# Performance work log

Measured on AMD Instinct MI355X. Metric: run time of the kernel, lower is better.

Reference implementation:

```python
import jax, jax.numpy as jnp
import numpy as np

V, E, H, B, TE, TD = 32000, 256, 256, 32, 128, 64


def _gru_cell(x, h, Wi, Wh, bi, bh):
    # PyTorch GRU gate order: r, z, n
    gi = x @ Wi.T + bi            # [B, 3H]
    gh = h @ Wh.T + bh            # [B, 3H]
    i_r, i_z, i_n = jnp.split(gi, 3, axis=-1)
    h_r, h_z, h_n = jnp.split(gh, 3, axis=-1)
    r = jax.nn.sigmoid(i_r + h_r)
    z = jax.nn.sigmoid(i_z + h_z)
    n = jnp.tanh(i_n + r * h_n)
    return (1.0 - z) * n + z * h


def _run_gru(x_seq, h0, Wi, Wh, bi, bh, reverse=False):
    # x_seq: [B, T, D] -> outputs [B, T, H]
    xs = jnp.swapaxes(x_seq, 0, 1)  # [T, B, D]
    def step(h, x_t):
        h = _gru_cell(x_t, h, Wi, Wh, bi, bh)
        return h, h
    _, ys = jax.lax.scan(step, h0, xs, reverse=reverse)
    return jnp.swapaxes(ys, 0, 1)


def setup_inputs() -> dict:
    key = jax.random.key(0)
    ks = jax.random.split(key, 22)
    k = 1.0 / np.sqrt(H)
    u = lambda kk, shape, a: jax.random.uniform(kk, shape, jnp.float32, -a, a)
    return {
        'enc_in': jax.random.randint(ks[0], (B, TE), 0, V),
        'dec_in': jax.random.randint(ks[1], (B, TD), 0, V),
        'embed_W': u(ks[2], (V, E), 0.1),
        'Wi_f': u(ks[3], (3 * H, E), k), 'Wh_f': u(ks[4], (3 * H, H), k),
        'bi_f': u(ks[5], (3 * H,), k), 'bh_f': u(ks[6], (3 * H,), k),
        'Wi_b': u(ks[7], (3 * H, E), k), 'Wh_b': u(ks[8], (3 * H, H), k),
        'bi_b': u(ks[9], (3 * H,), k), 'bh_b': u(ks[10], (3 * H,), k),
        'Wi_d': u(ks[11], (3 * H, E + 2 * H), k), 'Wh_d': u(ks[12], (3 * H, H), k),
        'bi_d': u(ks[13], (3 * H,), k), 'bh_d': u(ks[14], (3 * H,), k),
        'W1_w': u(ks[15], (H, 2 * H), 1.0 / np.sqrt(2 * H)), 'W1_b': u(ks[16], (H,), 1.0 / np.sqrt(2 * H)),
        'W2_w': u(ks[17], (2 * H, H), k), 'W2_b': u(ks[18], (2 * H,), k),
        'lin_w': u(ks[19], (V, H), 0.1), 'lin_b': jnp.zeros((V,), jnp.float32),
    }


def reference(enc_in, dec_in, embed_W, Wi_f, Wh_f, bi_f, bh_f, Wi_b, Wh_b, bi_b, bh_b,
              Wi_d, Wh_d, bi_d, bh_d, W1_w, W1_b, W2_w, W2_b, lin_w, lin_b):
    # ---- encoder (bidirectional GRU, 1 layer) ----
    enc_emb = embed_W[enc_in]                                   # [B, TE, E]
    h0 = jnp.zeros((B, H), enc_emb.dtype)
    out_f = _run_gru(enc_emb, h0, Wi_f, Wh_f, bi_f, bh_f)       # [B, TE, H]
    out_b = _run_gru(enc_emb, h0, Wi_b, Wh_b, bi_b, bh_b, reverse=True)
    encoded = jnp.concatenate([out_f, out_b], axis=-1)          # [B, TE, 2H]

    # last valid state per example: encoded[i, sizes[i]-1]
    sizes = (enc_in > 0).sum(axis=1)                            # [B]
    last_states = encoded[jnp.arange(B), sizes - 1]             # [B, 2H]

    # ---- decoder with Luong attention (teacher forcing) ----
    dec_emb = embed_W[dec_in]                                   # [B, TD, E]
    h_init = last_states @ W1_w.T + W1_b                        # [B, H]
    ctx_init = jnp.zeros((B, 2 * H), enc_emb.dtype)

    def dec_step(carry, x_t):
        h, ctx = carry
        inp = jnp.concatenate([ctx, x_t], axis=-1)              # [B, E+2H]
        h = _gru_cell(inp, h, Wi_d, Wh_d, bi_d, bh_d)           # [B, H]
        comp = h @ W2_w.T + W2_b                                # [B, 2H]
        scores = jax.nn.softmax(jnp.einsum('bte,be->bt', encoded, comp), axis=-1)
        ctx = jnp.einsum('bt,bte->be', scores, encoded)          # [B, 2H]
        return (h, ctx), h

    _, outs = jax.lax.scan(dec_step, (h_init, ctx_init), jnp.swapaxes(dec_emb, 0, 1))
    outs = jnp.swapaxes(outs, 0, 1)                             # [B, TD, H]
    logits = outs @ lin_w.T + lin_b                             # [B, TD, V]
    return logits
```

## Files before the change

### kernel.cpp

```cpp
#include <hip/hip_runtime.h>
#include <hip/hip_bf16.h>

#define Vv 32000
#define Ee 256
#define Hh 256
#define Bb 32
#define TEe 128
#define TDd 64

typedef __attribute__((ext_vector_type(4))) float f32x4;
typedef __attribute__((ext_vector_type(8))) short short8;
typedef __attribute__((ext_vector_type(2))) unsigned int uint2v;
typedef __attribute__((ext_vector_type(4))) unsigned int uint4v;

static __device__ __forceinline__ unsigned short f2bf(float f){
  unsigned u = __float_as_uint(f);
  u += 0x7fffu + ((u >> 16) & 1u);
  return (unsigned short)(u >> 16);
}
static __device__ __forceinline__ unsigned pack2(float a, float b){
  return ((unsigned)f2bf(b) << 16) | (unsigned)f2bf(a);
}
static __device__ __forceinline__ float dot8(uint4v u, const float* hh){
  float s = 0.f;
  #pragma unroll
  for (int i = 0; i < 4; ++i){
    unsigned w = u[i];
    s = fmaf(__uint_as_float(w << 16),        hh[2*i],   s);
    s = fmaf(__uint_as_float(w & 0xffff0000u), hh[2*i+1], s);
  }
  return s;
}
static __device__ __forceinline__ float sigmoidf_(float x){
  return 1.f / (1.f + __expf(-x));
}

__global__ void k_sizes(const int* __restrict__ enc_in, int* __restrict__ sizes){
  int b = threadIdx.x;
  if (b < Bb){
    int c = 0;
    for (int t = 0; t < TEe; ++t) c += (enc_in[b*TEe + t] > 0);
    sizes[b] = c;
  }
}

__global__ void k_gather(const int* __restrict__ tok, const float* __restrict__ embW,
                         unsigned short* __restrict__ out, int rows){
  int i = blockIdx.x * 256 + threadIdx.x;
  int r = i >> 8, c = i & 255;
  if (r < rows) out[i] = f2bf(embW[(size_t)tok[r]*Ee + c]);
}

__global__ void k_chunkw(const float* __restrict__ src, unsigned short* __restrict__ dst, int rows){
  int idx = blockIdx.x * 256 + threadIdx.x;
  if (idx < rows * 256){
    int i = idx & 7, r = (idx >> 3) % rows, kb = idx / (rows * 8);
    dst[idx] = f2bf(src[(size_t)r*256 + kb*8 + i]);
  }
}

__global__ void k_convert(const float* __restrict__ Wi_f, const float* __restrict__ Wi_b,
                          const float* __restrict__ Wi_d, const float* __restrict__ W2_w,
                          unsigned short* __restrict__ wif, unsigned short* __restrict__ wib,
                          unsigned short* __restrict__ wid, unsigned short* __restrict__ w2t){
  int idx = blockIdx.x * 256 + threadIdx.x;
  if (idx < 196608)        wif[idx] = f2bf(Wi_f[idx]);
  else if (idx < 393216)   wib[idx - 196608] = f2bf(Wi_b[idx - 196608]);
  else if (idx < 983040)   wid[idx - 393216] = f2bf(Wi_d[idx - 393216]);
  else if (idx < 1114112){
    int l = idx - 983040;
    int n = l >> 9, k = l & 511;
    w2t[l] = f2bf(W2_w[k*256 + n]);
  }
}

__global__ void k_projchunk(const unsigned short* __restrict__ in, unsigned short* __restrict__ out){
  int idx = blockIdx.x * 256 + threadIdx.x;
  int i = idx & 7;
  int t1 = idx >> 3;
  int n = t1 % 768;
  int t2 = t1 / 768;
  int kb = t2 & 15, b = t2 >> 4;
  out[idx] = in[(size_t)(b*TEe + kb*8 + i)*768 + n];
}

template<bool A_BF16, bool B_BF16, bool B_KMAJOR, bool OUT_BF16>
__global__ __launch_bounds__(256) void k_gemm(
  const void* __restrict__ Av, const void* __restrict__ Bv,
  const float* __restrict__ bias, void* __restrict__ Cv,
  int M, int N, int K, int lda, int ldb, int ldc)
{
  __shared__ unsigned short lA[128*40];
  __shared__ unsigned short lB[128*40];
  const int tid  = threadIdx.x;
  const int lane = tid & 63;
  const int w = tid >> 6, wr = w >> 1, wc = w & 1;
  const int m0 = blockIdx.y * 128, n0 = blockIdx.x * 128;
  f32x4 acc[4][4];
  #pragma unroll
  for (int i = 0; i < 4; ++i)
    #pragma unroll
    for (int j = 0; j < 4; ++j) acc[i][j] = (f32x4){0.f,0.f,0.f,0.f};

  for (int k0 = 0; k0 < K; k0 += 32){
    if (A_BF16){
      const unsigned short* A = (const unsigned short*)Av;
      #pragma unroll
      for (int it = 0; it < 2; ++it){
        int idx = tid + it*256; int r = idx >> 2, q = idx & 3;
        *(uint4v*)&lA[r*40 + q*8] = *(const uint4v*)(A + (size_t)(m0+r)*lda + k0 + q*8);
      }
    } else {
      const float* A = (const float*)Av;
      #pragma unroll
      for (int it = 0; it < 4; ++it){
        int idx = tid + it*256; int r = idx >> 3, q = idx & 7;
        f32x4 v = *(const f32x4*)(A + (size_t)(m0+r)*lda + k0 + q*4);
        uint2v pk; pk[0] = pack2(v[0], v[1]); pk[1] = pack2(v[2], v[3]);
        *(uint2v*)&lA[r*40 + q*4] = pk;
      }
    }
    if (B_KMAJOR){
      const float* Bp = (const float*)Bv;
      #pragma unroll
      for (int it = 0; it < 4; ++it){
        int idx = tid + it*256; int kk = idx >> 5, nq = idx & 31;
        f32x4 v = *(const f32x4*)(Bp + (size_t)(k0+kk)*ldb + n0 + nq*4);
        #pragma unroll
        for (int s2 = 0; s2 < 4; ++s2) lB[(nq*4+s2)*40 + kk] = f2bf(v[s2]);
      }
    } else if (B_BF16){
      const unsigned short* Bp = (const unsigned short*)Bv;
      #pragma unroll
      for (int it = 0; it < 2; ++it){
        int idx = tid + it*256; int r = idx >> 2, q = idx & 3;
        *(uint4v*)&lB[r*40 + q*8] = *(const uint4v*)(Bp + (size_t)(n0+r)*ldb + k0 + q*8);
      }
    } else {
      const float* Bp = (const float*)Bv;
      #pragma unroll
      for (int it = 0; it < 4; ++it){
        int idx = tid + it*256; int r = idx >> 3, q = idx & 7;
        f32x4 v = *(const f32x4*)(Bp + (size_t)(n0+r)*ldb + k0 + q*4);
        uint2v pk; pk[0] = pack2(v[0], v[1]); pk[1] = pack2(v[2], v[3]);
        *(uint2v*)&lB[r*40 + q*4] = pk;
      }
    }
    __syncthreads();
    short8 av[4], bv[4];
    #pragma unroll
    for (int i = 0; i < 4; ++i)
      av[i] = *(const short8*)&lA[(wr*64 + i*16 + (lane&15))*40 + (lane>>4)*8];
    #pragma unroll
    for (int j = 0; j < 4; ++j)
      bv[j] = *(const short8*)&lB[(wc*64 + j*16 + (lane&15))*40 + (lane>>4)*8];
    #pragma unroll
    for (int i = 0; i < 4; ++i)
      #pragma unroll
      for (int j = 0; j < 4; ++j)
        acc[i][j] = __builtin_amdgcn_mfma_f32_16x16x32_bf16(av[i], bv[j], acc[i][j], 0, 0, 0);
    __syncthreads();
  }
  #pragma unroll
  for (int i = 0; i < 4; ++i){
    #pragma unroll
    for (int j = 0; j < 4; ++j){
      int col = n0 + wc*64 + j*16 + (lane & 15);
      float bb = bias ? bias[col] : 0.f;
      #pragma unroll
      for (int r = 0; r < 4; ++r){
        int row = m0 + wr*64 + i*16 + (lane>>4)*4 + r;
        float v = acc[i][j][r] + bb;
        if (OUT_BF16) ((unsigned short*)Cv)[(size_t)row*ldc + col] = f2bf(v);
        else          ((float*)Cv)[(size_t)row*ldc + col] = v;
      }
    }
  }
}

__global__ __launch_bounds__(1024) void k_encoder(
  const unsigned short* __restrict__ Whf, const unsigned short* __restrict__ Whb,
  const float* __restrict__ bhf, const float* __restrict__ bhb,
  const float* __restrict__ gif, const float* __restrict__ gib,
  float* __restrict__ encoded, unsigned short* __restrict__ encoded_bf,
  const float* __restrict__ lin_w, unsigned short* __restrict__ lin_bf, int do_lin)
{
  if (blockIdx.x >= 64){
    if (do_lin){
      const int nlin = Vv*Hh;
      for (int i = (blockIdx.x - 64)*1024 + threadIdx.x; i < nlin; i += 128*1024)
        lin_bf[i] = f2bf(lin_w[i]);
    }
    return;
  }
  extern __shared__ char smem[];
  unsigned short* lw = (unsigned short*)smem;
  float* hA   = (float*)(smem + 131072);
  float* hB   = (float*)(smem + 132096);
  float* parA = (float*)(smem + 133120);
  float* parB = (float*)(smem + 137216);
  const int dir = blockIdx.x & 1, b = blockIdx.x >> 1;
  const unsigned short* Wh = dir ? Whb : Whf;
  const float* bh = dir ? bhb : bhf;
  const float* gi = dir ? gib : gif;
  const int T = threadIdx.x;
  const int rl = T & 255, q4 = T >> 8;
  const int rrh = T & 511, hf = T >> 9;
  const unsigned short* wsrc = Wh + (size_t)(hf*16)*6144 + (size_t)(256 + rrh)*8;
  uint4v wb[8];
  #pragma unroll
  for (int d = 0; d < 8; ++d) wb[d] = *(const uint4v*)(wsrc + (size_t)d*6144);
  for (int cc = T; cc < 256*32; cc += 1024){
    int r = cc >> 5, q = cc & 31;
    *(uint4v*)&lw[(r*32 + (q ^ (r & 31)))*8] = *(const uint4v*)(Wh + (size_t)q*6144 + r*8);
  }
  float bh0 = 0.f, bh1 = 0.f, bh2 = 0.f;
  if (T < 256){ bh0 = bh[T]; bh1 = bh[T+256]; bh2 = bh[T+512]; hA[T] = 0.f; }
  __syncthreads();
  const float* hc = hA; float* hn = hB;
  for (int s = 0; s < TEe; ++s){
    const int t = dir ? (TEe-1-s) : s;
    float aL = 0.f;
    #pragma unroll
    for (int i = 0; i < 8; ++i){
      const int ck = q4*8 + i;
      float hr[8];
      *(f32x4*)&hr[0] = *(const f32x4*)&hc[ck*8];
      *(f32x4*)&hr[4] = *(const f32x4*)&hc[ck*8+4];
      aL += dot8(*(const uint4v*)&lw[(rl*32 + (ck ^ (rl & 31)))*8], hr);
    }
    parA[q4*256 + rl] = aL;
    float aR = 0.f;
    const float* hh = hc + hf*128;
    #pragma unroll
    for (int q = 0; q < 16; ++q){
      float hr[8];
      *(f32x4*)&hr[0] = *(const f32x4*)&hh[q*8];
      *(f32x4*)&hr[4] = *(const f32x4*)&hh[q*8+4];
      aR += dot8(wb[q & 7], hr);
      wb[q & 7] = *(const uint4v*)(wsrc + (size_t)((q < 8) ? (q + 8) : (q - 8))*6144);
    }
    parB[hf*512 + rrh] = aR;
    __syncthreads();
    if (T < 256){
      const int j = T;
      const float* grow = gi + (size_t)(b*TEe + t)*768;
      const float A0 = parA[j] + parA[256+j] + parA[512+j] + parA[768+j] + bh0;
      const float A1 = parB[j] + parB[512+j] + bh1;
      const float A2 = parB[256+j] + parB[768+j] + bh2;
      const float r = sigmoidf_(grow[j] + A0);
      const float z = sigmoidf_(grow[j+256] + A1);
      const float n = tanhf(grow[j+512] + r*A2);
      const float hnew = (1.f - z)*n + z*hc[j];
      hn[j] = hnew;
      const size_t off = (size_t)(b*TEe + t)*512 + dir*256 + j;
      encoded[off] = hnew;
      encoded_bf[off] = f2bf(hnew);
    }
    __syncthreads();
    const float* tmp = hc; hc = hn; hn = (float*)tmp;
  }
}

__global__ void k_encb2(const float* __restrict__ encoded, const float* __restrict__ W2b,
                        float* __restrict__ encb2){
  int r = blockIdx.x, l = threadIdx.x;
  const float* e = encoded + (size_t)r*512;
  float s = 0.f;
  for (int k = l; k < 512; k += 64) s += e[k]*W2b[k];
  for (int off = 32; off; off >>= 1) s += __shfl_down(s, off);
  if (l == 0) encb2[r] = s;
}

__global__ void k_hinit(const float* __restrict__ encoded, const int* __restrict__ sizes,
                        const float* __restrict__ W1w, const float* __restrict__ W1b,
                        float* __restrict__ h0){
  int b = blockIdx.x, o = threadIdx.x;
  int idx = sizes[b] - 1;
  idx = idx < 0 ? 0 : (idx > TEe-1 ? TEe-1 : idx);
  const float* ls = encoded + (size_t)(b*TEe + idx)*512;
  const float* wv = W1w + (size_t)o*512;
  float s = W1b[o];
  for (int k = 0; k < 512; k += 4){
    f32x4 a = *(const f32x4*)(ls + k);
    f32x4 w4 = *(const f32x4*)(wv + k);
    s = fmaf(a[0],w4[0], fmaf(a[1],w4[1], fmaf(a[2],w4[2], fmaf(a[3],w4[3], s))));
  }
  h0[b*256 + o] = s;
}

#define DLR 128
__global__ __launch_bounds__(512, 1) void k_decoder(
  const unsigned short* __restrict__ Whd, const float* __restrict__ bhd,
  const float* __restrict__ gidx,
  const unsigned short* __restrict__ encw2,
  const float* __restrict__ encb2,
  const unsigned short* __restrict__ projt,
  const float* __restrict__ h0,
  unsigned short* __restrict__ outs_bf)
{
  extern __shared__ char smem[];
  unsigned short* le = (unsigned short*)smem;
  unsigned short* lw = (unsigned short*)(smem + 65536);
  float* h    = (float*)(smem + 131072);
  float* parL = (float*)(smem + 132096);
  float* parS1= (float*)(smem + 134144);
  float* parS2= (float*)(smem + 136192);
  float* gcs  = (float*)(smem + 138240);
  float* cpar = (float*)(smem + 140288);
  float* p    = (float*)(smem + 142336);
  float* ebl  = (float*)(smem + 142848);
  const int b = blockIdx.x, T = threadIdx.x;
  const unsigned short* ptc = projt + (size_t)b*98304;
  const unsigned short* wsrcM = Whd + (size_t)(DLR + T)*8;
  const int trow = 640 + (T >> 2), tq = (T & 3)*8;
  const unsigned short* wsrcT = Whd + (size_t)trow*8;
  const unsigned short* csrcM = ptc + (size_t)T*8;
  const int crow = 512 + (T >> 1), cq = (T & 1)*8;
  const unsigned short* csrcT = ptc + (size_t)crow*8;
  uint4v wb[8], wb2[2], cb[4], cb2[2];
  #pragma unroll
  for (int d = 0; d < 8; ++d) wb[d] = *(const uint4v*)(wsrcM + (size_t)d*6144);
  wb2[0] = *(const uint4v*)(wsrcT + (size_t)tq*6144);
  wb2[1] = *(const uint4v*)(wsrcT + (size_t)(tq+1)*6144);
  #pragma unroll
  for (int d = 0; d < 4; ++d) cb[d] = *(const uint4v*)(csrcM + (size_t)d*6144);
  cb2[0] = *(const uint4v*)(csrcT + (size_t)cq*6144);
  cb2[1] = *(const uint4v*)(csrcT + (size_t)(cq+1)*6144);
  for (int cc = T; cc < 128*32; cc += 512){
    int r = cc >> 5, q = cc & 31;
    *(uint4v*)&le[(r*32 + (q ^ (r & 31)))*8] =
        *(const uint4v*)(encw2 + ((size_t)(b*TEe + r) << 8) + (q << 3));
  }
  for (int cc = T; cc < DLR*32; cc += 512){
    int r = cc >> 5, q = cc & 31;
    *(uint4v*)&lw[(r*32 + (q ^ (r & 31)))*8] =
        *(const uint4v*)(Whd + (size_t)q*6144 + r*8);
  }
  for (int i = T; i < 256; i += 512) h[i] = h0[b*256 + i];
  gcs[T] = 0.f; cpar[T] = 0.f;
  if (T < TEe) ebl[T] = encb2[b*TEe + T];
  float bh0 = 0.f, bh1 = 0.f, bh2 = 0.f;
  if (T < 256){ bh0 = bhd[T]; bh1 = bhd[T+256]; bh2 = bhd[T+512]; }
  __syncthreads();
  float g0 = 0.f, g1 = 0.f, g2 = 0.f;
  if (T < 256){
    const float* grow = gidx + (size_t)(b*TDd)*768;
    g0 = grow[T]; g1 = grow[T+256]; g2 = grow[T+512];
  }
  #define DOTS_BODY                                                            \
  {                                                                            \
    { const int rL2 = T >> 2, qb2 = (T & 3)*8;                                 \
      const unsigned short* lwr = lw + rL2*256;                                \
      float a = 0.f;                                                           \
      _Pragma("unroll")                                                        \
      for (int i = 0; i < 8; ++i){                                             \
        const int q = qb2 + i;                                                 \
        float hr[8];                                                           \
        *(f32x4*)&hr[0] = *(const f32x4*)&h[q*8];                              \
        *(f32x4*)&hr[4] = *(const f32x4*)&h[q*8+4];                            \
        a += dot8(*(const uint4v*)(lwr + ((q ^ (rL2 & 31)) << 3)), hr);        \
      }                                                                        \
      parL[(T & 3)*128 + rL2] = a;                                             \
    }                                                                          \
    { float a = 0.f;                                                           \
      _Pragma("unroll")                                                        \
      for (int q = 0; q < 32; ++q){                                            \
        float hr[8];                                                           \
        *(f32x4*)&hr[0] = *(const f32x4*)&h[q*8];                              \
        *(f32x4*)&hr[4] = *(const f32x4*)&h[q*8+4];                            \
        a += dot8(wb[q & 7], hr);                                              \
        wb[q & 7] = *(const uint4v*)(wsrcM + (size_t)((q < 24) ? (q + 8) : (q - 24))*6144); \
      }                                                                        \
      parS1[T] = a;                                                            \
    }                                                                          \
    { float a = 0.f;                                                           \
      _Pragma("unroll")                                                        \
      for (int i = 0; i < 8; ++i){                                             \
        const int q = tq + i;                                                  \
        float hr[8];                                                           \
        *(f32x4*)&hr[0] = *(const f32x4*)&h[q*8];                              \
        *(f32x4*)&hr[4] = *(const f32x4*)&h[q*8+4];                            \
        a += dot8(wb2[i & 1], hr);                                             \
        wb2[i & 1] = *(const uint4v*)(wsrcT + (size_t)(tq + ((i < 6) ? (i + 2) : (i - 6)))*6144); \
      }                                                                        \
      parS2[(T & 3)*128 + (T >> 2)] = a;                                       \
    }                                                                          \
  }
  DOTS_BODY
  __syncthreads();
  for (int t = 0; t < TDd; ++t){
    if (T < 256){
      const int j = T;
      float A0, A2;
      if (j < 128){
        A0 = parL[j] + parL[128+j] + parL[256+j] + parL[384+j];
        A2 = parS1[384+j];
      } else {
        A0 = parS1[j-128];
        A2 = parS2[j-128] + parS2[j] + parS2[j+128] + parS2[j+256];
      }
      const float A1 = parS1[128+j];
      const float gcr = gcs[j];
      const float gcz = gcs[256+j];
      const float gcn = cpar[j] + cpar[256+j];
      const float r = sigmoidf_(g0 + gcr + A0 + bh0);
      const float z = sigmoidf_(g1 + gcz + A1 + bh1);
      const float n = tanhf(g2 + gcn + r*(A2 + bh2));
      const float hnew = (1.f - z)*n + z*h[j];
      h[j] = hnew;
      outs_bf[(size_t)(b*TDd + t)*256 + j] = f2bf(hnew);
    }
    if (t + 1 == TDd) break;
    __syncthreads();
    if (T < 256){
      const float* grow = gidx + (size_t)(b*TDd + t + 1)*768;
      g0 = grow[T]; g1 = grow[T+256]; g2 = grow[T+512];
    }
    DOTS_BODY
    {
      const int pos = T >> 2, kq = (T & 3)*8;
      const unsigned short* er = le + pos*256;
      float s = 0.f;
      #pragma unroll
      for (int i = 0; i < 8; ++i){
        const int q = kq + i;
        float hr[8];
        *(f32x4*)&hr[0] = *(const f32x4*)&h[q*8];
        *(f32x4*)&hr[4] = *(const f32x4*)&h[q*8+4];
        s += dot8(*(const uint4v*)(er + ((q ^ (pos & 31)) << 3)), hr);
      }
      s += __shfl_xor(s, 1);
      s += __shfl_xor(s, 2);
      if ((T & 3) == 0) p[pos] = s + ebl[pos];
    }
    __syncthreads();
    if (T < 64){
      float m = fmaxf(p[T], p[T+64]);
      for (int off = 32; off; off >>= 1) m = fmaxf(m, __shfl_xor(m, off));
      float e0 = __expf(p[T] - m), e1 = __expf(p[T+64] - m);
      float ss = e0 + e1;
      for (int off = 32; off; off >>= 1) ss += __shfl_xor(ss, off);
      float inv = 1.f / ss;
      p[T] = e0*inv; p[T+64] = e1*inv;
    }
    __syncthreads();
    {
      float c = 0.f;
      #pragma unroll
      for (int q = 0; q < 16; ++q){
        float pr[8];
        *(f32x4*)&pr[0] = *(const f32x4*)&p[q*8];
        *(f32x4*)&pr[4] = *(const f32x4*)&p[q*8+4];
        c += dot8(cb[q & 3], pr);
        cb[q & 3] = *(const uint4v*)(csrcM + (size_t)((q < 12) ? (q + 4) : (q - 12))*6144);
      }
      gcs[T] = c;
      float c2 = 0.f;
      #pragma unroll
      for (int i = 0; i < 8; ++i){
        const int q = cq + i;
        float pr[8];
        *(f32x4*)&pr[0] = *(const f32x4*)&p[q*8];
        *(f32x4*)&pr[4] = *(const f32x4*)&p[q*8+4];
        c2 += dot8(cb2[i & 1], pr);
        cb2[i & 1] = *(const uint4v*)(csrcT + (size_t)(cq + ((i < 6) ? (i + 2) : (i - 6)))*6144);
      }
      cpar[(T & 1)*256 + (T >> 1)] = c2;
    }
    __syncthreads();
  }
  #undef DOTS_BODY
}

extern "C" void kernel_launch(void* const* d_in, const int* in_sizes, int n_in,
                              void* d_out, int out_size, void* d_ws, size_t ws_size,
                              hipStream_t stream)
{
  (void)in_sizes; (void)n_in; (void)out_size;
  const int*   enc_in = (const int*)d_in[0];
  const int*   dec_in = (const int*)d_in[1];
  const float* embW   = (const float*)d_in[2];
  const float* Wi_f   = (const float*)d_in[3];
  const float* Wh_f   = (const float*)d_in[4];
  const float* bi_f   = (const float*)d_in[5];
  const float* bh_f   = (const float*)d_in[6];
  const float* Wi_b   = (const float*)d_in[7];
  const float* Wh_b   = (const float*)d_in[8];
  const float* bi_b   = (const float*)d_in[9];
  const float* bh_b   = (const float*)d_in[10];
  const float* Wi_d   = (const float*)d_in[11];
  const float* Wh_d   = (const float*)d_in[12];
  const float* bi_d   = (const float*)d_in[13];
  const float* bh_d   = (const float*)d_in[14];
  const float* W1_w   = (const float*)d_in[15];
  const float* W1_b   = (const float*)d_in[16];
  const float* W2_w   = (const float*)d_in[17];
  const float* W2_b   = (const float*)d_in[18];
  const float* lin_w  = (const float*)d_in[19];
  const float* lin_b  = (const float*)d_in[20];

  char* scr = (char*)d_out;
  unsigned short* emb_enc = (unsigned short*)(scr + 0);
  unsigned short* emb_dec = (unsigned short*)(scr + 2097152);
  float* gi_f    = (float*)(scr + 3145728);
  float* gi_b    = (float*)(scr + 15728640);
  float* gi_dx   = (float*)(scr + 28311552);
  float* enc     = (float*)(scr + 34603008);
  unsigned short* enc_bf  = (unsigned short*)(scr + 42991616);
  unsigned short* projf_bf= (unsigned short*)(scr + 47185920);
  unsigned short* whf_bf = (unsigned short*)(scr + 53477376);
  unsigned short* whb_bf = (unsigned short*)(scr + 53870592);
  unsigned short* whd_bf = (unsigned short*)(scr + 54263808);
  unsigned short* encw2  = (unsigned short*)(scr + 54657024);
  unsigned short* projt  = (unsigned short*)(scr + 56754176);
  unsigned short* wif_bf = (unsigned short*)(scr + 63045632);
  unsigned short* wib_bf = (unsigned short*)(scr + 63438848);
  unsigned short* wid_bf = (unsigned short*)(scr + 63832064);
  unsigned short* w2t_bf = (unsigned short*)(scr + 65011712);
  float* encb2 = (float*)(scr + 65273856);
  int*   sizes = (int*)(scr + 65290240);
  float* h0    = (float*)(scr + 65290368);

  unsigned short* outs_bf = (unsigned short*)d_ws;
  unsigned short* lin_bf  = (unsigned short*)((char*)d_ws + (1<<20));
  const bool big = ws_size >= (size_t)(1<<20) + 16384000u + 1024u;

  hipFuncSetAttribute((const void*)k_encoder, hipFuncAttributeMaxDynamicSharedMemorySize, 141312);
  hipFuncSetAttribute((const void*)k_decoder, hipFuncAttributeMaxDynamicSharedMemorySize, 143360);

  k_sizes<<<1, 32, 0, stream>>>(enc_in, sizes);
  k_gather<<<Bb*TEe, 256, 0, stream>>>(enc_in, embW, emb_enc, Bb*TEe);
  k_gather<<<Bb*TDd, 256, 0, stream>>>(dec_in, embW, emb_dec, Bb*TDd);
  k_chunkw<<<768, 256, 0, stream>>>(Wh_f, whf_bf, 768);
  k_chunkw<<<768, 256, 0, stream>>>(Wh_b, whb_bf, 768);
  k_chunkw<<<768, 256, 0, stream>>>(Wh_d, whd_bf, 768);
  k_convert<<<4352, 256, 0, stream>>>(Wi_f, Wi_b, Wi_d, W2_w, wif_bf, wib_bf, wid_bf, w2t_bf);

  k_gemm<true,true,false,false><<<dim3(6,32), 256, 0, stream>>>(
      emb_enc, wif_bf, bi_f, gi_f, 4096, 768, 256, 256, 256, 768);
  k_gemm<true,true,false,false><<<dim3(6,32), 256, 0, stream>>>(
      emb_enc, wib_bf, bi_b, gi_b, 4096, 768, 256, 256, 256, 768);
  k_gemm<true,true,false,false><<<dim3(6,16), 256, 0, stream>>>(
      emb_dec, wid_bf + 512, bi_d, gi_dx, 2048, 768, 256, 256, 768, 768);

  k_encoder<<<192, 1024, 141312, stream>>>(whf_bf, whb_bf, bh_f, bh_b, gi_f, gi_b,
                                           enc, enc_bf, lin_w, lin_bf, big ? 1 : 0);
  k_encb2<<<Bb*TEe, 64, 0, stream>>>(enc, W2_b, encb2);

  k_gemm<true,true,false,true><<<dim3(2,32), 256, 0, stream>>>(
      enc_bf, w2t_bf, nullptr, encw2, 4096, 256, 512, 512, 512, 256);
  k_gemm<true,true,false,true><<<dim3(6,32), 256, 0, stream>>>(
      enc_bf, wid_bf, nullptr, projf_bf, 4096, 768, 512, 512, 768, 768);
  k_projchunk<<<(Bb*16*768*8)/256, 256, 0, stream>>>(projf_bf, projt);
  k_hinit<<<Bb, 256, 0, stream>>>(enc, sizes, W1_w, W1_b, h0);

  k_decoder<<<Bb, 512, 143360, stream>>>(whd_bf, bh_d, gi_dx, encw2, encb2, projt, h0, outs_bf);

  if (big)
    k_gemm<true,true,false,false><<<dim3(250,16), 256, 0, stream>>>(
        outs_bf, lin_bf, lin_b, d_out, 2048, 32000, 256, 256, 256, 32000);
  else
    k_gemm<true,false,false,false><<<dim3(250,16), 256, 0, stream>>>(
        outs_bf, lin_w, lin_b, d_out, 2048, 32000, 256, 256, 256, 32000);
}
```

Measured before the change: 1.650 ms.

## Fuse prep kernels, embedding gather into GEMM, and chunked projection output

Measured after the change: 1.624 ms, median of 2. No clear change (-1.6%).

```diff
diff --git a/kernel.cpp b/kernel.cpp
--- a/kernel.cpp
+++ b/kernel.cpp
@@ -35,58 +35,35 @@
   return 1.f / (1.f + __expf(-x));
 }
 
-__global__ void k_sizes(const int* __restrict__ enc_in, int* __restrict__ sizes){
-  int b = threadIdx.x;
-  if (b < Bb){
-    int c = 0;
-    for (int t = 0; t < TEe; ++t) c += (enc_in[b*TEe + t] > 0);
-    sizes[b] = c;
-  }
-}
-
-__global__ void k_gather(const int* __restrict__ tok, const float* __restrict__ embW,
-                         unsigned short* __restrict__ out, int rows){
-  int i = blockIdx.x * 256 + threadIdx.x;
-  int r = i >> 8, c = i & 255;
-  if (r < rows) out[i] = f2bf(embW[(size_t)tok[r]*Ee + c]);
-}
-
-__global__ void k_chunkw(const float* __restrict__ src, unsigned short* __restrict__ dst, int rows){
+__global__ void k_prep(const float* __restrict__ Wh_f, const float* __restrict__ Wh_b,
+                       const float* __restrict__ Wh_d,
+                       const float* __restrict__ Wi_f, const float* __restrict__ Wi_b,
+                       const float* __restrict__ Wi_d, const float* __restrict__ W2_w,
+                       unsigned short* __restrict__ whf, unsigned short* __restrict__ whb,
+                       unsigned short* __restrict__ whd,
+                       unsigned short* __restrict__ wif, unsigned short* __restrict__ wib,
+                       unsigned short* __restrict__ wid, unsigned short* __restrict__ w2t){
   int idx = blockIdx.x * 256 + threadIdx.x;
-  if (idx < rows * 256){
-    int i = idx & 7, r = (idx >> 3) % rows, kb = idx / (rows * 8);
-    dst[idx] = f2bf(src[(size_t)r*256 + kb*8 + i]);
-  }
-}
-
-__global__ void k_convert(const float* __restrict__ Wi_f, const float* __restrict__ Wi_b,
-                          const float* __restrict__ Wi_d, const float* __restrict__ W2_w,
-                          unsigned short* __restrict__ wif, unsigned short* __restrict__ wib,
-                          unsigned short* __restrict__ wid, unsigned short* __restrict__ w2t){
-  int idx = blockIdx.x * 256 + threadIdx.x;
-  if (idx < 196608)        wif[idx] = f2bf(Wi_f[idx]);
-  else if (idx < 393216)   wib[idx - 196608] = f2bf(Wi_b[idx - 196608]);
-  else if (idx < 983040)   wid[idx - 393216] = f2bf(Wi_d[idx - 393216]);
-  else if (idx < 1114112){
-    int l = idx - 983040;
+  if (idx < 589824){
+    int which = idx / 196608, local = idx % 196608;
+    int i = local & 7, r = (local >> 3) % 768, kb = local / 6144;
+    const float* src = (which == 0) ? Wh_f : (which == 1) ? Wh_b : Wh_d;
+    unsigned short* dst = (which == 0) ? whf : (which == 1) ? whb : whd;
+    dst[local] = f2bf(src[(size_t)r*256 + kb*8 + i]);
+  } else if (idx < 786432)   wif[idx - 589824] = f2bf(Wi_f[idx - 589824]);
+  else if (idx < 983040)     wib[idx - 786432] = f2bf(Wi_b[idx - 786432]);
+  else if (idx < 1572864)    wid[idx - 983040] = f2bf(Wi_d[idx - 983040]);
+  else if (idx < 1703936){
+    int l = idx - 1572864;
     int n = l >> 9, k = l & 511;
     w2t[l] = f2bf(W2_w[k*256 + n]);
   }
 }
 
-__global__ void k_projchunk(const unsigned short* __restrict__ in, unsigned short* __restrict__ out){
-  int idx = blockIdx.x * 256 + threadIdx.x;
-  int i = idx & 7;
-  int t1 = idx >> 3;
-  int n = t1 % 768;
-  int t2 = t1 / 768;
-  int kb = t2 & 15, b = t2 >> 4;
-  out[idx] = in[(size_t)(b*TEe + kb*8 + i)*768 + n];
-}
-
-template<bool A_BF16, bool B_BF16, bool B_KMAJOR, bool OUT_BF16>
+template<bool A_BF16, bool A_GATHER, bool B_BF16, int OUTMODE>
 __global__ __launch_bounds__(256) void k_gemm(
-  const void* __restrict__ Av, const void* __restrict__ Bv,
+  const void* __restrict__ Av, const int* __restrict__ tokp, const float* __restrict__ embp,
+  const void* __restrict__ Bv,
   const float* __restrict__ bias, void* __restrict__ Cv,
   int M, int N, int K, int lda, int ldb, int ldc)
 {
@@ -103,7 +80,16 @@
     for (int j = 0; j < 4; ++j) acc[i][j] = (f32x4){0.f,0.f,0.f,0.f};
 
   for (int k0 = 0; k0 < K; k0 += 32){
-    if (A_BF16){
+    if (A_GATHER){
+      #pragma unroll
+      for (int it = 0; it < 4; ++it){
+        int idx = tid + it*256; int r = idx >> 3, q = idx & 7;
+        const float* src = embp + (size_t)tokp[m0 + r]*256 + k0 + q*4;
+        f32x4 v = *(const f32x4*)src;
+        uint2v pk; pk[0] = pack2(v[0], v[1]); pk[1] = pack2(v[2], v[3]);
+        *(uint2v*)&lA[r*40 + q*4] = pk;
+      }
+    } else if (A_BF16){
       const unsigned short* A = (const unsigned short*)Av;
       #pragma unroll
       for (int it = 0; it < 2; ++it){
@@ -120,16 +106,7 @@
         *(uint2v*)&lA[r*40 + q*4] = pk;
       }
     }
-    if (B_KMAJOR){
-      const float* Bp = (const float*)Bv;
-      #pragma unroll
-      for (int it = 0; it < 4; ++it){
-        int idx = tid + it*256; int kk = idx >> 5, nq = idx & 31;
-        f32x4 v = *(const f32x4*)(Bp + (size_t)(k0+kk)*ldb + n0 + nq*4);
-        #pragma unroll
-        for (int s2 = 0; s2 < 4; ++s2) lB[(nq*4+s2)*40 + kk] = f2bf(v[s2]);
-      }
-    } else if (B_BF16){
+    if (B_BF16){
       const unsigned short* Bp = (const unsigned short*)Bv;
       #pragma unroll
       for (int it = 0; it < 2; ++it){
@@ -171,8 +148,14 @@
       for (int r = 0; r < 4; ++r){
         int row = m0 + wr*64 + i*16 + (lane>>4)*4 + r;
         float v = acc[i][j][r] + bb;
-        if (OUT_BF16) ((unsigned short*)Cv)[(size_t)row*ldc + col] = f2bf(v);
-        else          ((float*)Cv)[(size_t)row*ldc + col] = v;
+        if (OUTMODE == 2){
+          ((unsigned short*)Cv)[(size_t)(row >> 7)*98304 + (size_t)((row & 127) >> 3)*6144
+                                + (size_t)col*8 + (row & 7)] = f2bf(v);
+        } else if (OUTMODE == 1){
+          ((unsigned short*)Cv)[(size_t)row*ldc + col] = f2bf(v);
+        } else {
+          ((float*)Cv)[(size_t)row*ldc + col] = v;
+        }
       }
     }
   }
@@ -220,6 +203,11 @@
   const float* hc = hA; float* hn = hB;
   for (int s = 0; s < TEe; ++s){
     const int t = dir ? (TEe-1-s) : s;
+    float g0 = 0.f, g1 = 0.f, g2 = 0.f;
+    if (T < 256){
+      const float* grow = gi + (size_t)(b*TEe + t)*768;
+      g0 = grow[T]; g1 = grow[T+256]; g2 = grow[T+512];
+    }
     float aL = 0.f;
     #pragma unroll
     for (int i = 0; i < 8; ++i){
@@ -244,13 +232,12 @@
     __syncthreads();
     if (T < 256){
       const int j = T;
-      const float* grow = gi + (size_t)(b*TEe + t)*768;
       const float A0 = parA[j] + parA[256+j] + parA[512+j] + parA[768+j] + bh0;
       const float A1 = parB[j] + parB[512+j] + bh1;
       const float A2 = parB[256+j] + parB[768+j] + bh2;
-      const float r = sigmoidf_(grow[j] + A0);
-      const float z = sigmoidf_(grow[j+256] + A1);
-      const float n = tanhf(grow[j+512] + r*A2);
+      const float r = sigmoidf_(g0 + A0);
+      const float z = sigmoidf_(g1 + A1);
+      const float n = tanhf(g2 + r*A2);
       const float hnew = (1.f - z)*n + z*hc[j];
       hn[j] = hnew;
       const size_t off = (size_t)(b*TEe + t)*512 + dir*256 + j;
@@ -262,31 +249,34 @@
   }
 }
 
-__global__ void k_encb2(const float* __restrict__ encoded, const float* __restrict__ W2b,
-                        float* __restrict__ encb2){
-  int r = blockIdx.x, l = threadIdx.x;
-  const float* e = encoded + (size_t)r*512;
-  float s = 0.f;
-  for (int k = l; k < 512; k += 64) s += e[k]*W2b[k];
-  for (int off = 32; off; off >>= 1) s += __shfl_down(s, off);
-  if (l == 0) encb2[r] = s;
-}
-
-__global__ void k_hinit(const float* __restrict__ encoded, const int* __restrict__ sizes,
-                        const float* __restrict__ W1w, const float* __restrict__ W1b,
-                        float* __restrict__ h0){
-  int b = blockIdx.x, o = threadIdx.x;
-  int idx = sizes[b] - 1;
-  idx = idx < 0 ? 0 : (idx > TEe-1 ? TEe-1 : idx);
-  const float* ls = encoded + (size_t)(b*TEe + idx)*512;
-  const float* wv = W1w + (size_t)o*512;
-  float s = W1b[o];
-  for (int k = 0; k < 512; k += 4){
-    f32x4 a = *(const f32x4*)(ls + k);
-    f32x4 w4 = *(const f32x4*)(wv + k);
-    s = fmaf(a[0],w4[0], fmaf(a[1],w4[1], fmaf(a[2],w4[2], fmaf(a[3],w4[3], s))));
-  }
-  h0[b*256 + o] = s;
+__global__ __launch_bounds__(256) void k_post(
+  const float* __restrict__ encoded, const float* __restrict__ W2b, float* __restrict__ encb2,
+  const int* __restrict__ enc_in, const float* __restrict__ W1w, const float* __restrict__ W1b,
+  float* __restrict__ h0)
+{
+  if (blockIdx.x < 1024){
+    const int r = blockIdx.x*4 + (threadIdx.x >> 6), l = threadIdx.x & 63;
+    const float* e = encoded + (size_t)r*512;
+    float s = 0.f;
+    for (int k = l; k < 512; k += 64) s += e[k]*W2b[k];
+    for (int off = 32; off; off >>= 1) s += __shfl_down(s, off);
+    if (l == 0) encb2[r] = s;
+  } else {
+    const int b = blockIdx.x - 1024, o = threadIdx.x;
+    int c = 0;
+    for (int t = 0; t < TEe; ++t) c += (enc_in[b*TEe + t] > 0);
+    int idx = c - 1;
+    idx = idx < 0 ? 0 : (idx > TEe-1 ? TEe-1 : idx);
+    const float* ls = encoded + (size_t)(b*TEe + idx)*512;
+    const float* wv = W1w + (size_t)o*512;
+    float s = W1b[o];
+    for (int k = 0; k < 512; k += 4){
+      f32x4 a = *(const f32x4*)(ls + k);
+      f32x4 w4 = *(const f32x4*)(wv + k);
+      s = fmaf(a[0],w4[0], fmaf(a[1],w4[1], fmaf(a[2],w4[2], fmaf(a[3],w4[3], s))));
+    }
+    h0[b*256 + o] = s;
+  }
 }
 
 #define DLR 128
@@ -501,14 +491,11 @@
   const float* lin_b  = (const float*)d_in[20];
 
   char* scr = (char*)d_out;
-  unsigned short* emb_enc = (unsigned short*)(scr + 0);
-  unsigned short* emb_dec = (unsigned short*)(scr + 2097152);
   float* gi_f    = (float*)(scr + 3145728);
   float* gi_b    = (float*)(scr + 15728640);
   float* gi_dx   = (float*)(scr + 28311552);
   float* enc     = (float*)(scr + 34603008);
   unsigned short* enc_bf  = (unsigned short*)(scr + 42991616);
-  unsigned short* projf_bf= (unsigned short*)(scr + 47185920);
   unsigned short* whf_bf = (unsigned short*)(scr + 53477376);
   unsigned short* whb_bf = (unsigned short*)(scr + 53870592);
   unsigned short* whd_bf = (unsigned short*)(scr + 54263808);
@@ -519,7 +506,6 @@
   unsigned short* wid_bf = (unsigned short*)(scr + 63832064);
   unsigned short* w2t_bf = (unsigned short*)(scr + 65011712);
   float* encb2 = (float*)(scr + 65273856);
-  int*   sizes = (int*)(scr + 65290240);
   float* h0    = (float*)(scr + 65290368);
 
   unsigned short* outs_bf = (unsigned short*)d_ws;
@@ -529,38 +515,31 @@
   hipFuncSetAttribute((const void*)k_encoder, hipFuncAttributeMaxDynamicSharedMemorySize, 141312);
   hipFuncSetAttribute((const void*)k_decoder, hipFuncAttributeMaxDynamicSharedMemorySize, 143360);
 
-  k_sizes<<<1, 32, 0, stream>>>(enc_in, sizes);
-  k_gather<<<Bb*TEe, 256, 0, stream>>>(enc_in, embW, emb_enc, Bb*TEe);
-  k_gather<<<Bb*TDd, 256, 0, stream>>>(dec_in, embW, emb_dec, Bb*TDd);
-  k_chunkw<<<768, 256, 0, stream>>>(Wh_f, whf_bf, 768);
-  k_chunkw<<<768, 256, 0, stream>>>(Wh_b, whb_bf, 768);
-  k_chunkw<<<768, 256, 0, stream>>>(Wh_d, whd_bf, 768);
-  k_convert<<<4352, 256, 0, stream>>>(Wi_f, Wi_b, Wi_d, W2_w, wif_bf, wib_bf, wid_bf, w2t_bf);
-
-  k_gemm<true,true,false,false><<<dim3(6,32), 256, 0, stream>>>(
-      emb_enc, wif_bf, bi_f, gi_f, 4096, 768, 256, 256, 256, 768);
-  k_gemm<true,true,false,false><<<dim3(6,32), 256, 0, stream>>>(
-      emb_enc, wib_bf, bi_b, gi_b, 4096, 768, 256, 256, 256, 768);
-  k_gemm<true,true,false,false><<<dim3(6,16), 256, 0, stream>>>(
-      emb_dec, wid_bf + 512, bi_d, gi_dx, 2048, 768, 256, 256, 768, 768);
+  k_prep<<<6656, 256, 0, stream>>>(Wh_f, Wh_b, Wh_d, Wi_f, Wi_b, Wi_d, W2_w,
+                                   whf_bf, whb_bf, whd_bf, wif_bf, wib_bf, wid_bf, w2t_bf);
+
+  k_gemm<false,true,true,0><<<dim3(6,32), 256, 0, stream>>>(
+      nullptr, enc_in, embW, wif_bf, bi_f, gi_f, 4096, 768, 256, 0, 256, 768);
+  k_gemm<false,true,true,0><<<dim3(6,32), 256, 0, stream>>>(
+      nullptr, enc_in, embW, wib_bf, bi_b, gi_b, 4096, 768, 256, 0, 256, 768);
+  k_gemm<false,true,true,0><<<dim3(6,16), 256, 0, stream>>>(
+      nullptr, dec_in, embW, wid_bf + 512, bi_d, gi_dx, 2048, 768, 256, 0, 768, 768);
 
   k_encoder<<<192, 1024, 141312, stream>>>(whf_bf, whb_bf, bh_f, bh_b, gi_f, gi_b,
                                            enc, enc_bf, lin_w, lin_bf, big ? 1 : 0);
-  k_encb2<<<Bb*TEe, 64, 0, stream>>>(enc, W2_b, encb2);
-
-  k_gemm<true,true,false,true><<<dim3(2,32), 256, 0, stream>>>(
-      enc_bf, w2t_bf, nullptr, encw2, 4096, 256, 512, 512, 512, 256);
-  k_gemm<true,true,false,true><<<dim3(6,32), 256, 0, stream>>>(
-      enc_bf, wid_bf, nullptr, projf_bf, 4096, 768, 512, 512, 768, 768);
-  k_projchunk<<<(Bb*16*768*8)/256, 256, 0, stream>>>(projf_bf, projt);
-  k_hinit<<<Bb, 256, 0, stream>>>(enc, sizes, W1_w, W1_b, h0);
+  k_post<<<1056, 256, 0, stream>>>(enc, W2_b, encb2, enc_in, W1_w, W1_b, h0);
+
+  k_gemm<true,false,true,1><<<dim3(2,32), 256, 0, stream>>>(
+      enc_bf, nullptr, nullptr, w2t_bf, nullptr, encw2, 4096, 256, 512, 512, 512, 256);
+  k_gemm<true,false,true,2><<<dim3(6,32), 256, 0, stream>>>(
+      enc_bf, nullptr, nullptr, wid_bf, nullptr, projt, 4096, 768, 512, 512, 768, 0);
 
   k_decoder<<<Bb, 512, 143360, stream>>>(whd_bf, bh_d, gi_dx, encw2, encb2, projt, h0, outs_bf);
 
   if (big)
-    k_gemm<true,true,false,false><<<dim3(250,16), 256, 0, stream>>>(
-        outs_bf, lin_bf, lin_b, d_out, 2048, 32000, 256, 256, 256, 32000);
+    k_gemm<true,false,true,0><<<dim3(250,16), 256, 0, stream>>>(
+        outs_bf, nullptr, nullptr, lin_bf, lin_b, d_out, 2048, 32000, 256, 256, 256, 32000);
   else
-    k_gemm<true,false,false,false><<<dim3(250,16), 256, 0, stream>>>(
-        outs_bf, lin_w, lin_b, d_out, 2048, 32000, 256, 256, 256, 32000);
-}
+    k_gemm<true,false,false,0><<<dim3(250,16), 256, 0, stream>>>(
+        outs_bf, nullptr, nullptr, lin_w, lin_b, d_out, 2048, 32000, 256, 256, 256, 32000);
+}
```
